# Performance work log

Hardware: AMD Instinct MI355X
Metric: run time of the kernel (lower is better)

## Reference

```python
import jax, jax.numpy as jnp
import numpy as np

DIM_MODEL = 512
DIM_HEAD = 64


def setup_inputs() -> dict:
    key = jax.random.key(0)
    ks = jax.random.split(key, 7)
    B, S = 4, 4096
    scale = 1.0 / np.sqrt(DIM_MODEL)
    x = jax.random.normal(ks[0], (B, S, DIM_MODEL), dtype=jnp.float32)
    # nn.Linear weights: stored as [out, in] in torch; we use [in, out] for x @ W
    Wq = jax.random.uniform(ks[1], (DIM_MODEL, DIM_HEAD), jnp.float32, -scale, scale)
    Wk = jax.random.uniform(ks[2], (DIM_MODEL, DIM_HEAD), jnp.float32, -scale, scale)
    Wv = jax.random.uniform(ks[3], (DIM_MODEL, DIM_HEAD), jnp.float32, -scale, scale)
    bq = jax.random.uniform(ks[4], (DIM_HEAD,), jnp.float32, -scale, scale)
    bk = jax.random.uniform(ks[5], (DIM_HEAD,), jnp.float32, -scale, scale)
    bv = jax.random.uniform(ks[6], (DIM_HEAD,), jnp.float32, -scale, scale)
    return {"x": x, "Wq": Wq, "bq": bq, "Wk": Wk, "bk": bk, "Wv": Wv, "bv": bv}


def reference(x, Wq, bq, Wk, bk, Wv, bv):
    # [q,k,v] = z @ U_qkv
    q = x @ Wq + bq  # [B, S, Dh]
    k = x @ Wk + bk
    v = x @ Wv + bv
    dot_scale = jnp.sqrt(jnp.asarray(DIM_HEAD, dtype=x.dtype))
    scores = jnp.einsum("bsd,btd->bst", q, k) / dot_scale  # [B, S, S]
    attn = jax.nn.softmax(scores, axis=-1)
    return jnp.einsum("bst,btd->bsd", attn, v)  # [B, S, Dh]
```

## Files before the change

### kernel.cpp

```cpp
#include <hip/hip_runtime.h>
#include <hip/hip_bf16.h>

typedef short short8 __attribute__((ext_vector_type(8)));
typedef float f32x4 __attribute__((ext_vector_type(4)));

#define MFMA16(a,b,c) __builtin_amdgcn_mfma_f32_16x16x32_bf16((a),(b),(c),0,0,0)

#define NROWS 16384
#define LOG2E 1.44269504088896340736f

#define OFF_Q  0u
#define OFF_K  (2u<<20)
#define OFF_V  (4u<<20)
#define OFF_W  (6u<<20)
#define OFF_O  ((6u<<20) + (1u<<18))

__device__ __forceinline__ unsigned short f2bf(float f){
    union { float f; unsigned u; } v; v.f = f;
    unsigned r = v.u + 0x7FFFu + ((v.u >> 16) & 1u);
    return (unsigned short)(r >> 16);
}
__device__ __forceinline__ unsigned pk2(float a, float b){
    union { __hip_bfloat162 h; unsigned u; } c;
    c.h = __float22bfloat162_rn(make_float2(a, b));
    return c.u;
}

union Frag {
    short8 s;
    unsigned short u[8];
    uint2 d2[2];
    uint4 q4;
};

__global__ __launch_bounds__(256) void wprep_kernel(
    const float* __restrict__ Wq, const float* __restrict__ Wk,
    const float* __restrict__ Wv, unsigned short* __restrict__ wfrag)
{
    int idx = blockIdx.x * 256 + threadIdx.x;
    int lane = idx & 63;
    int rest = idx >> 6;
    int kk = rest & 15;
    int nt = (rest >> 4) & 3;
    int w  = rest >> 6;
    const float* W = (w == 0) ? Wq : (w == 1) ? Wk : Wv;
    float scl = (w == 0) ? (0.125f * LOG2E) : 1.0f;
    int n = 16 * nt + (lane & 15);
    int g = lane >> 4;
    Frag o;
#pragma unroll
    for (int e = 0; e < 8; ++e) {
        int k = 32 * kk + 16 * (e >> 2) + 4 * g + (e & 3);
        o.u[e] = f2bf(W[k * 64 + n] * scl);
    }
    *(uint4*)(wfrag + (size_t)idx * 8) = o.q4;
}

__global__ __launch_bounds__(192) void qkv_kernel(
    const float* __restrict__ x,
    const float* __restrict__ bq, const float* __restrict__ bk,
    const float* __restrict__ bv,
    const unsigned short* __restrict__ wfrag,
    unsigned short* __restrict__ qfrag,
    unsigned short* __restrict__ kfrag,
    unsigned short* __restrict__ vfrag)
{
    __shared__ unsigned short xs[16][520];
    const int tid = threadIdx.x;
    const int lane = tid & 63;
    const int w = tid >> 6;
    const int l15 = lane & 15, g = lane >> 4;
    const int rg = blockIdx.x;
    const float* xbase = x + (size_t)rg * 16 * 512;

    for (int i = tid; i < 2048; i += 192) {
        float4 v = *(const float4*)(xbase + i * 4);
        int r_ = i >> 7;
        int c_ = (i & 127) * 4;
        *(uint2*)&xs[r_][c_] = make_uint2(pk2(v.x, v.y), pk2(v.z, v.w));
    }
    __syncthreads();

    f32x4 acc[4];
#pragma unroll
    for (int nt = 0; nt < 4; ++nt) acc[nt] = (f32x4){0.f,0.f,0.f,0.f};

    const uint4* wf = (const uint4*)wfrag + (size_t)w * 4096;

#pragma unroll
    for (int kk = 0; kk < 16; ++kk) {
        Frag xf;
        xf.d2[0] = *(const uint2*)&xs[l15][32 * kk + 4 * g];
        xf.d2[1] = *(const uint2*)&xs[l15][32 * kk + 16 + 4 * g];

        Frag wr[4];
#pragma unroll
        for (int nt = 0; nt < 4; ++nt)
            wr[nt].q4 = wf[((size_t)nt * 16 + kk) * 64 + lane];

        if (w == 2) {
#pragma unroll
            for (int nt = 0; nt < 4; ++nt) acc[nt] = MFMA16(xf.s, wr[nt].s, acc[nt]);
        } else {
#pragma unroll
            for (int nt = 0; nt < 4; ++nt) acc[nt] = MFMA16(wr[nt].s, xf.s, acc[nt]);
        }
    }

    const int b   = rg >> 8;
    const int rgb = rg & 255;
    const int tc  = rgb >> 2;
    const int c   = rgb & 3;

    if (w == 0) {
#pragma unroll
        for (int nt = 0; nt < 4; ++nt) {
            float4 bb = *(const float4*)(bq + 16 * nt + 4 * g);
            const float bs = 0.125f * LOG2E;
            float q0 = acc[nt][0] + bb.x * bs;
            float q1 = acc[nt][1] + bb.y * bs;
            float q2 = acc[nt][2] + bb.z * bs;
            float q3 = acc[nt][3] + bb.w * bs;
            int ks = nt >> 1, h = nt & 1;
            size_t qoff = ((size_t)(rg * 2 + ks) * 64 + lane) * 8 + h * 4;
            *(uint2*)(qfrag + qoff) = make_uint2(pk2(q0, q1), pk2(q2, q3));
        }
    } else if (w == 1) {
#pragma unroll
        for (int nt = 0; nt < 4; ++nt) {
            float4 bb = *(const float4*)(bk + 16 * nt + 4 * g);
            float k0 = acc[nt][0] + bb.x;
            float k1 = acc[nt][1] + bb.y;
            float k2 = acc[nt][2] + bb.z;
            float k3 = acc[nt][3] + bb.w;
            int ks = nt >> 1, h = nt & 1;
            size_t kfi = ((size_t)((b * 64 + tc) * 4 + c) * 2 + ks);
            size_t koff = (kfi * 64 + lane) * 8 + h * 4;
            *(uint2*)(kfrag + koff) = make_uint2(pk2(k0, k1), pk2(k2, k3));
        }
    } else {
        const int vks = c >> 1, vh = c & 1;
#pragma unroll
        for (int nt = 0; nt < 4; ++nt) {
            float bvv = bv[16 * nt + l15];
            float v0 = acc[nt][0] + bvv;
            float v1 = acc[nt][1] + bvv;
            float v2 = acc[nt][2] + bvv;
            float v3 = acc[nt][3] + bvv;
            size_t vfi = ((size_t)((b * 64 + tc) * 4 + nt) * 2 + vks);
            size_t voff = (vfi * 64 + lane) * 8 + vh * 4;
            *(uint2*)(vfrag + voff) = make_uint2(pk2(v0, v1), pk2(v2, v3));
        }
    }
}

#define LOADKV(KD, VD, CH) do { \
    const size_t b_ = ((size_t)(tcg0 + (CH)) * 8) * 64 + lane; \
    _Pragma("unroll") \
    for (int c_ = 0; c_ < 4; ++c_) { \
        KD[c_][0].q4 = kf4[b_ + (size_t)(c_ * 2 + 0) * 64]; \
        KD[c_][1].q4 = kf4[b_ + (size_t)(c_ * 2 + 1) * 64]; \
        VD[c_][0].q4 = vf4[b_ + (size_t)(c_ * 2 + 0) * 64]; \
        VD[c_][1].q4 = vf4[b_ + (size_t)(c_ * 2 + 1) * 64]; \
    } } while (0)

#define BODY(KC, VC, KN, VN, CHN) do { \
    LOADKV(KN, VN, CHN); \
    _Pragma("unroll") \
    for (int M_ = 0; M_ < 2; ++M_) { \
        f32x4 sD[4]; \
        _Pragma("unroll") \
        for (int c_ = 0; c_ < 4; ++c_) { \
            f32x4 D = (f32x4){0.f,0.f,0.f,0.f}; \
            D = MFMA16(KC[c_][0].s, qf[M_][0].s, D); \
            D = MFMA16(KC[c_][1].s, qf[M_][1].s, D); \
            sD[c_] = D; \
        } \
        Frag pa0, pa1; \
        float lloc = 0.f; \
        _Pragma("unroll") \
        for (int c_ = 0; c_ < 4; ++c_) { \
            float p0 = __builtin_exp2f(sD[c_][0]); \
            float p1 = __builtin_exp2f(sD[c_][1]); \
            float p2 = __builtin_exp2f(sD[c_][2]); \
            float p3 = __builtin_exp2f(sD[c_][3]); \
            lloc += (p0 + p1) + (p2 + p3); \
            uint2 pk_ = make_uint2(pk2(p0, p1), pk2(p2, p3)); \
            if (c_ < 2) pa0.d2[c_ & 1] = pk_; else pa1.d2[c_ & 1] = pk_; \
        } \
        l_run[M_] += lloc; \
        _Pragma("unroll") \
        for (int dc_ = 0; dc_ < 4; ++dc_) { \
            acc[M_][dc_] = MFMA16(pa0.s, VC[dc_][0].s, acc[M_][dc_]); \
            acc[M_][dc_] = MFMA16(pa1.s, VC[dc_][1].s, acc[M_][dc_]); \
        } \
    } } while (0)

__global__ __launch_bounds__(256, 2) void attn_kernel(
    const unsigned short* __restrict__ qfrag,
    const unsigned short* __restrict__ kfrag,
    const unsigned short* __restrict__ vfrag,
    uint2* __restrict__ OpartU, float* __restrict__ lml,
    int CPS, int SBITS)
{
    const int tid = threadIdx.x;
    const int lane = tid & 63;
    const int w = tid >> 6;
    const int l15 = lane & 15, g = lane >> 4;
    const int split  = blockIdx.x & ((1 << SBITS) - 1);
    const int qblock = blockIdx.x >> SBITS;
    const int gw = qblock * 4 + w;
    const int b = gw >> 7;
    const int tcg0 = b * 64 + split * CPS;

    const uint4* qf4 = (const uint4*)qfrag;
    const uint4* kf4 = (const uint4*)kfrag;
    const uint4* vf4 = (const uint4*)vfrag;

    Frag qf[2][2];
#pragma unroll
    for (int M = 0; M < 2; ++M)
#pragma unroll
        for (int ks = 0; ks < 2; ++ks)
            qf[M][ks].q4 = qf4[((size_t)((gw * 2 + M) * 2 + ks)) * 64 + lane];

    f32x4 acc[2][4];
#pragma unroll
    for (int M = 0; M < 2; ++M)
#pragma unroll
        for (int dc = 0; dc < 4; ++dc) acc[M][dc] = (f32x4){0.f,0.f,0.f,0.f};
    float l_run[2] = {0.f, 0.f};

    Frag kA[4][2], kB[4][2], vA[4][2], vB[4][2];
    LOADKV(kA, vA, 0);

#pragma unroll 1
    for (int ch = 0; ch < CPS; ch += 2) {
        int c1 = (ch + 1 < CPS) ? (ch + 1) : ch;
        int c2 = (ch + 2 < CPS) ? (ch + 2) : ch;
        BODY(kA, vA, kB, vB, c1);
        BODY(kB, vB, kA, vA, c2);
    }

#pragma unroll
    for (int M = 0; M < 2; ++M) {
        float lt = l_run[M];
        lt += __shfl_xor(lt, 16);
        lt += __shfl_xor(lt, 32);
#pragma unroll
        for (int dc = 0; dc < 4; ++dc)
            OpartU[((size_t)(split * 512 + gw) * 8 + M * 4 + dc) * 64 + lane] =
                make_uint2(pk2(acc[M][dc][0], acc[M][dc][1]),
                           pk2(acc[M][dc][2], acc[M][dc][3]));
        if (g == 0)
            lml[(size_t)(split * 512 + gw) * 32 + M * 16 + l15] = lt;
    }
}

__global__ __launch_bounds__(256) void merge_kernel(
    const uint2* __restrict__ OpartU, const float* __restrict__ lml,
    float* __restrict__ out, int S)
{
    int gid = blockIdx.x * 256 + threadIdx.x;
    int lane = gid & 63;
    int dc = (gid >> 6) & 3;
    int M  = (gid >> 8) & 1;
    int gw = gid >> 9;
    int l15 = lane & 15, g = lane >> 4;

    float o0 = 0.f, o1 = 0.f, o2 = 0.f, o3 = 0.f;
    float L0 = 0.f, L1 = 0.f, L2 = 0.f, L3 = 0.f;
    for (int s = 0; s < S; ++s) {
        uint2 pv = OpartU[((size_t)(s * 512 + gw) * 8 + M * 4 + dc) * 64 + lane];
        float4 lv = *(const float4*)(lml + (size_t)(s * 512 + gw) * 32 + M * 16 + 4 * g);
        o0 += __uint_as_float(pv.x << 16);
        o1 += __uint_as_float(pv.x & 0xFFFF0000u);
        o2 += __uint_as_float(pv.y << 16);
        o3 += __uint_as_float(pv.y & 0xFFFF0000u);
        L0 += lv.x; L1 += lv.y; L2 += lv.z; L3 += lv.w;
    }
    size_t row = (size_t)gw * 32 + M * 16 + 4 * g;
    int col = 16 * dc + l15;
    out[(row + 0) * 64 + col] = o0 / L0;
    out[(row + 1) * 64 + col] = o1 / L1;
    out[(row + 2) * 64 + col] = o2 / L2;
    out[(row + 3) * 64 + col] = o3 / L3;
}

extern "C" void kernel_launch(void* const* d_in, const int* in_sizes, int n_in,
                              void* d_out, int out_size, void* d_ws, size_t ws_size,
                              hipStream_t stream) {
    (void)in_sizes; (void)n_in; (void)out_size;
    const float* x  = (const float*)d_in[0];
    const float* Wq = (const float*)d_in[1];
    const float* bq = (const float*)d_in[2];
    const float* Wk = (const float*)d_in[3];
    const float* bk = (const float*)d_in[4];
    const float* Wv = (const float*)d_in[5];
    const float* bv = (const float*)d_in[6];
    float* out = (float*)d_out;

    char* ws = (char*)d_ws;
    unsigned short* qfrag = (unsigned short*)(ws + OFF_Q);
    unsigned short* kfrag = (unsigned short*)(ws + OFF_K);
    unsigned short* vfrag = (unsigned short*)(ws + OFF_V);
    unsigned short* wfrag = (unsigned short*)(ws + OFF_W);

    const size_t oneO = (size_t)512 * 8 * 64 * 8;
    const size_t oneL = (size_t)512 * 32 * 4;
    int S = 8, SBITS = 3;
    if (ws_size < (size_t)OFF_O + 8 * (oneO + oneL)) { S = 4; SBITS = 2; }
    if (ws_size < (size_t)OFF_O + 4 * (oneO + oneL)) { S = 2; SBITS = 1; }
    uint2* OpartU = (uint2*)(ws + OFF_O);
    float* lml    = (float*)(ws + OFF_O + (size_t)S * oneO);
    int CPS = 64 / S;

    hipLaunchKernelGGL(wprep_kernel, dim3(48), dim3(256), 0, stream,
                       Wq, Wk, Wv, wfrag);
    hipLaunchKernelGGL(qkv_kernel, dim3(1024), dim3(192), 0, stream,
                       x, bq, bk, bv, wfrag, qfrag, kfrag, vfrag);
    hipLaunchKernelGGL(attn_kernel, dim3(128 * S), dim3(256), 0, stream,
                       qfrag, kfrag, vfrag, OpartU, lml, CPS, SBITS);
    hipLaunchKernelGGL(merge_kernel, dim3(1024), dim3(256), 0, stream,
                       OpartU, lml, out, S);
}
```

Measured before the change: 69.25 us.

## Restructure K/V prefetch and double-buffer QKV weight loads with scheduling hints

In the attention kernel, V fragments are no longer prefetched a chunk ahead. They are loaded at the start of the current chunk, and only K is double-buffered. This cuts live registers, possibly to ease register pressure at two blocks per SIMD. MFMA sections get s_setprio raised, and sched_barriers pin where loads are issued. The QKV projection kernel now double-buffers its weight-fragment loads across pairs of k-steps. The risk is exposed V load latency, since V must arrive before the PV MFMAs of the same chunk.

Result: faster. 60.38 us (-12.8%).

```diff
diff --git a/kernel.cpp b/kernel.cpp
--- a/kernel.cpp
+++ b/kernel.cpp
@@ -55,6 +55,24 @@
     }
     *(uint4*)(wfrag + (size_t)idx * 8) = o.q4;
 }
+
+#define LDW(WD, KK) do { \
+    _Pragma("unroll") \
+    for (int nt_ = 0; nt_ < 4; ++nt_) \
+        WD[nt_].q4 = wf[((size_t)(nt_ * 16 + (KK))) * 64 + lane]; \
+    } while (0)
+
+#define DOK(WC, KK) do { \
+    Frag xf_; \
+    xf_.d2[0] = *(const uint2*)&xs[l15][32 * (KK) + 4 * g]; \
+    xf_.d2[1] = *(const uint2*)&xs[l15][32 * (KK) + 16 + 4 * g]; \
+    if (w == 2) { \
+        _Pragma("unroll") \
+        for (int nt_ = 0; nt_ < 4; ++nt_) acc[nt_] = MFMA16(xf_.s, WC[nt_].s, acc[nt_]); \
+    } else { \
+        _Pragma("unroll") \
+        for (int nt_ = 0; nt_ < 4; ++nt_) acc[nt_] = MFMA16(WC[nt_].s, xf_.s, acc[nt_]); \
+    } } while (0)
 
 __global__ __launch_bounds__(192) void qkv_kernel(
     const float* __restrict__ x,
@@ -87,24 +105,16 @@
 
     const uint4* wf = (const uint4*)wfrag + (size_t)w * 4096;
 
-#pragma unroll
-    for (int kk = 0; kk < 16; ++kk) {
-        Frag xf;
-        xf.d2[0] = *(const uint2*)&xs[l15][32 * kk + 4 * g];
-        xf.d2[1] = *(const uint2*)&xs[l15][32 * kk + 16 + 4 * g];
-
-        Frag wr[4];
-#pragma unroll
-        for (int nt = 0; nt < 4; ++nt)
-            wr[nt].q4 = wf[((size_t)nt * 16 + kk) * 64 + lane];
-
-        if (w == 2) {
-#pragma unroll
-            for (int nt = 0; nt < 4; ++nt) acc[nt] = MFMA16(xf.s, wr[nt].s, acc[nt]);
-        } else {
-#pragma unroll
-            for (int nt = 0; nt < 4; ++nt) acc[nt] = MFMA16(wr[nt].s, xf.s, acc[nt]);
-        }
+    Frag wA[4], wB[4];
+    LDW(wA, 0);
+#pragma unroll
+    for (int kp = 0; kp < 8; ++kp) {
+        LDW(wB, 2 * kp + 1);
+        __builtin_amdgcn_sched_barrier(0);
+        DOK(wA, 2 * kp);
+        if (2 * kp + 2 < 16) LDW(wA, 2 * kp + 2);
+        __builtin_amdgcn_sched_barrier(0);
+        DOK(wB, 2 * kp + 1);
     }
 
     const int b   = rg >> 8;
@@ -154,21 +164,31 @@
     }
 }
 
-#define LOADKV(KD, VD, CH) do { \
+#define LOADK(KD, CH) do { \
     const size_t b_ = ((size_t)(tcg0 + (CH)) * 8) * 64 + lane; \
     _Pragma("unroll") \
     for (int c_ = 0; c_ < 4; ++c_) { \
         KD[c_][0].q4 = kf4[b_ + (size_t)(c_ * 2 + 0) * 64]; \
         KD[c_][1].q4 = kf4[b_ + (size_t)(c_ * 2 + 1) * 64]; \
+    } } while (0)
+
+#define LOADV(VD, CH) do { \
+    const size_t b_ = ((size_t)(tcg0 + (CH)) * 8) * 64 + lane; \
+    _Pragma("unroll") \
+    for (int c_ = 0; c_ < 4; ++c_) { \
         VD[c_][0].q4 = vf4[b_ + (size_t)(c_ * 2 + 0) * 64]; \
         VD[c_][1].q4 = vf4[b_ + (size_t)(c_ * 2 + 1) * 64]; \
     } } while (0)
 
-#define BODY(KC, VC, KN, VN, CHN) do { \
-    LOADKV(KN, VN, CHN); \
+#define BODY(KC, KN, CH, CHN) do { \
+    Frag vC[4][2]; \
+    LOADV(vC, CH); \
+    LOADK(KN, CHN); \
+    __builtin_amdgcn_sched_barrier(0); \
     _Pragma("unroll") \
     for (int M_ = 0; M_ < 2; ++M_) { \
         f32x4 sD[4]; \
+        __builtin_amdgcn_s_setprio(1); \
         _Pragma("unroll") \
         for (int c_ = 0; c_ < 4; ++c_) { \
             f32x4 D = (f32x4){0.f,0.f,0.f,0.f}; \
@@ -176,6 +196,7 @@
             D = MFMA16(KC[c_][1].s, qf[M_][1].s, D); \
             sD[c_] = D; \
         } \
+        __builtin_amdgcn_s_setprio(0); \
         Frag pa0, pa1; \
         float lloc = 0.f; \
         _Pragma("unroll") \
@@ -189,11 +210,13 @@
             if (c_ < 2) pa0.d2[c_ & 1] = pk_; else pa1.d2[c_ & 1] = pk_; \
         } \
         l_run[M_] += lloc; \
+        __builtin_amdgcn_s_setprio(1); \
         _Pragma("unroll") \
         for (int dc_ = 0; dc_ < 4; ++dc_) { \
-            acc[M_][dc_] = MFMA16(pa0.s, VC[dc_][0].s, acc[M_][dc_]); \
-            acc[M_][dc_] = MFMA16(pa1.s, VC[dc_][1].s, acc[M_][dc_]); \
+            acc[M_][dc_] = MFMA16(pa0.s, vC[dc_][0].s, acc[M_][dc_]); \
+            acc[M_][dc_] = MFMA16(pa1.s, vC[dc_][1].s, acc[M_][dc_]); \
         } \
+        __builtin_amdgcn_s_setprio(0); \
     } } while (0)
 
 __global__ __launch_bounds__(256, 2) void attn_kernel(
@@ -231,15 +254,15 @@
         for (int dc = 0; dc < 4; ++dc) acc[M][dc] = (f32x4){0.f,0.f,0.f,0.f};
     float l_run[2] = {0.f, 0.f};
 
-    Frag kA[4][2], kB[4][2], vA[4][2], vB[4][2];
-    LOADKV(kA, vA, 0);
+    Frag kA[4][2], kB[4][2];
+    LOADK(kA, 0);
 
 #pragma unroll 1
     for (int ch = 0; ch < CPS; ch += 2) {
         int c1 = (ch + 1 < CPS) ? (ch + 1) : ch;
         int c2 = (ch + 2 < CPS) ? (ch + 2) : ch;
-        BODY(kA, vA, kB, vB, c1);
-        BODY(kB, vB, kA, vA, c2);
+        BODY(kA, kB, ch, c1);
+        BODY(kB, kA, c1, c2);
     }
 
 #pragma unroll
```
